# Performance work log

Hardware: AMD Instinct MI355X
Metric: run time of the kernel (lower is better)

## Reference

```python
import jax, jax.numpy as jnp
import numpy as np

H = 2048
S = 8192

def setup_inputs() -> dict:
    key = jax.random.key(0)
    k1, k2, k3 = jax.random.split(key, 3)
    hidden = jax.random.normal(k1, (1, 1, H), dtype=jnp.float32)
    encoder_outputs = jax.random.normal(k2, (S, 1, H), dtype=jnp.float32)
    # nn.Linear(H, H): weight [H, H], bias [H]; Kaiming-uniform-ish scale
    bound = 1.0 / np.sqrt(H)
    W = jax.random.uniform(k3, (H, H), dtype=jnp.float32, minval=-bound, maxval=bound)
    b = jnp.zeros((H,), dtype=jnp.float32)
    return {"hidden": hidden, "encoder_outputs": encoder_outputs, "W": W, "b": b}

def reference(hidden, encoder_outputs, W, b):
    # hidden: [1,1,H] -> [H]; encoder_outputs: [S,1,H] -> [S,H]
    h = hidden[0, 0]
    enc = encoder_outputs[:, 0, :]
    # per-step: energy_i = W @ enc_i + b; score_i = h . energy_i  (vectorized)
    energies = jnp.einsum('sh,h->s', enc @ W.T + b, h)  # [S]
    attn = jax.nn.softmax(energies)  # softmax over seq dim (dim 0 of 1-D tensor)
    return attn[None, None, :]  # [1,1,S]
```

## Files before the change

kernel.cpp:

```cpp
#include <hip/hip_runtime.h>
#include <math.h>

#define H 2048
#define S 8192
#define JCHUNK 64

__global__ void wt_h_kernel(const float* __restrict__ W, const float* __restrict__ h,
                            float* __restrict__ u) {
    int k = blockIdx.x * blockDim.x + threadIdx.x;
    int j0 = blockIdx.y * JCHUNK;
    float acc = 0.f;
#pragma unroll 8
    for (int j = j0; j < j0 + JCHUNK; ++j) {
        acc += h[j] * W[(size_t)j * H + k];
    }
    atomicAdd(&u[k], acc);
}

__global__ void enc_dot_kernel(const float* __restrict__ enc, const float* __restrict__ u,
                               float* __restrict__ e) {
    int wave = threadIdx.x >> 6;
    int lane = threadIdx.x & 63;
    int s = blockIdx.x * 4 + wave;
    const float4* row = (const float4*)(enc + (size_t)s * H);
    const float4* u4  = (const float4*)u;
    float acc = 0.f;
#pragma unroll
    for (int i = lane; i < H / 4; i += 64) {
        float4 a = row[i];
        float4 b = u4[i];
        acc += a.x * b.x + a.y * b.y + a.z * b.z + a.w * b.w;
    }
#pragma unroll
    for (int off = 32; off > 0; off >>= 1) acc += __shfl_down(acc, off);
    if (lane == 0) e[s] = acc;
}

__global__ void softmax_kernel(const float* __restrict__ e, float* __restrict__ out) {
    __shared__ float red[16];
    __shared__ float bcast;
    int tid = threadIdx.x;
    int lane = tid & 63;
    int wv = tid >> 6;

    float vals[8];
    float m = -INFINITY;
#pragma unroll
    for (int i = 0; i < 8; ++i) {
        vals[i] = e[tid + i * 1024];
        m = fmaxf(m, vals[i]);
    }
#pragma unroll
    for (int off = 32; off > 0; off >>= 1) m = fmaxf(m, __shfl_down(m, off));
    if (lane == 0) red[wv] = m;
    __syncthreads();
    if (tid == 0) {
        float mm = red[0];
#pragma unroll
        for (int i = 1; i < 16; ++i) mm = fmaxf(mm, red[i]);
        bcast = mm;
    }
    __syncthreads();
    float M = bcast;

    float ssum = 0.f;
#pragma unroll
    for (int i = 0; i < 8; ++i) {
        vals[i] = __expf(vals[i] - M);
        ssum += vals[i];
    }
#pragma unroll
    for (int off = 32; off > 0; off >>= 1) ssum += __shfl_down(ssum, off);
    if (lane == 0) red[wv] = ssum;
    __syncthreads();
    if (tid == 0) {
        float t = 0.f;
#pragma unroll
        for (int i = 0; i < 16; ++i) t += red[i];
        bcast = t;
    }
    __syncthreads();
    float inv = 1.f / bcast;
#pragma unroll
    for (int i = 0; i < 8; ++i) out[tid + i * 1024] = vals[i] * inv;
}

extern "C" void kernel_launch(void* const* d_in, const int* in_sizes, int n_in,
                              void* d_out, int out_size, void* d_ws, size_t ws_size,
                              hipStream_t stream) {
    const float* hidden = (const float*)d_in[0];
    const float* enc    = (const float*)d_in[1];
    const float* W      = (const float*)d_in[2];
    float* out = (float*)d_out;

    float* u = (float*)d_ws;
    float* e = (float*)((char*)d_ws + H * sizeof(float));

    hipMemsetAsync(u, 0, H * sizeof(float), stream);

    dim3 g1(H / 256, H / JCHUNK);
    wt_h_kernel<<<g1, 256, 0, stream>>>(W, hidden, u);

    enc_dot_kernel<<<S / 4, 256, 0, stream>>>(enc, u, e);

    softmax_kernel<<<1, 1024, 0, stream>>>(e, out);
}
```

Before: 114.2 us.

## Fuse all stages into one cooperative kernel with grid syncs and online softmax

Replaces the memset plus three kernel launches with a single cooperative kernel of 1024 blocks. Stage one computes partial W^T·h slices into a buffer, avoiding atomics; a second stage reduces them. Each block then computes 8 encoder dot products and a local max and exp-sum, and a final stage combines all block partials to normalise. This removes launch gaps and the single-block softmax, at the cost of three grid-wide barriers and a co-residency requirement (falls back to the old path if the cooperative launch fails).

New measurement: 411.6 us. 3.6x slower.

```diff
diff --git a/kernel.cpp b/kernel.cpp
--- a/kernel.cpp
+++ b/kernel.cpp
@@ -1,8 +1,116 @@
 #include <hip/hip_runtime.h>
+#include <hip/hip_cooperative_groups.h>
 #include <math.h>
 
 #define H 2048
 #define S 8192
+#define NBLK 1024
+#define NSLICE 128
+#define JCH (H / NSLICE)
+
+namespace cg = cooperative_groups;
+
+__global__ __launch_bounds__(256, 4)
+void fused_attn(const float* __restrict__ W, const float* __restrict__ h,
+                const float* __restrict__ enc, float* __restrict__ out,
+                float* __restrict__ u_part, float* __restrict__ u,
+                float* __restrict__ red) {
+    cg::grid_group grid = cg::this_grid();
+    const int b    = blockIdx.x;
+    const int tid  = threadIdx.x;
+    const int lane = tid & 63;
+    const int wave = tid >> 6;
+
+    __shared__ float evals[8];
+    __shared__ float wred[4];
+    __shared__ float bc[2];
+
+    {
+        const int kx = b & 7;
+        const int js = b >> 3;
+        const int k  = kx * 256 + tid;
+        const int j0 = js * JCH;
+        float acc = 0.f;
+#pragma unroll
+        for (int j = j0; j < j0 + JCH; ++j)
+            acc += h[j] * W[(size_t)j * H + k];
+        u_part[(size_t)js * H + k] = acc;
+    }
+    grid.sync();
+
+    {
+        const int t = b * 256 + tid;
+        if (t < H) {
+            float acc = 0.f;
+#pragma unroll 8
+            for (int js = 0; js < NSLICE; ++js)
+                acc += u_part[(size_t)js * H + t];
+            u[t] = acc;
+        }
+    }
+    grid.sync();
+
+    {
+        const float4* u4 = (const float4*)u;
+        for (int r = wave; r < 8; r += 4) {
+            const int s = b * 8 + r;
+            const float4* row = (const float4*)(enc + (size_t)s * H);
+            float acc = 0.f;
+#pragma unroll
+            for (int it = 0; it < 8; ++it) {
+                float4 a  = row[lane + it * 64];
+                float4 bb = u4 [lane + it * 64];
+                acc += a.x * bb.x + a.y * bb.y + a.z * bb.z + a.w * bb.w;
+            }
+#pragma unroll
+            for (int off = 32; off > 0; off >>= 1) acc += __shfl_down(acc, off);
+            if (lane == 0) evals[r] = acc;
+        }
+        __syncthreads();
+        if (tid == 0) {
+            float m = evals[0];
+#pragma unroll
+            for (int i = 1; i < 8; ++i) m = fmaxf(m, evals[i]);
+            float sb = 0.f;
+#pragma unroll
+            for (int i = 0; i < 8; ++i) sb += __expf(evals[i] - m);
+            red[2 * b]     = m;
+            red[2 * b + 1] = sb;
+        }
+    }
+    grid.sync();
+
+    {
+        float m4[4], s4[4];
+        float mt = -INFINITY;
+#pragma unroll
+        for (int q = 0; q < 4; ++q) {
+            const int i = tid + q * 256;
+            m4[q] = red[2 * i];
+            s4[q] = red[2 * i + 1];
+            mt = fmaxf(mt, m4[q]);
+        }
+#pragma unroll
+        for (int off = 32; off > 0; off >>= 1) mt = fmaxf(mt, __shfl_down(mt, off));
+        if (lane == 0) wred[wave] = mt;
+        __syncthreads();
+        if (tid == 0) bc[0] = fmaxf(fmaxf(wred[0], wred[1]), fmaxf(wred[2], wred[3]));
+        __syncthreads();
+        const float M = bc[0];
+        float st = 0.f;
+#pragma unroll
+        for (int q = 0; q < 4; ++q) st += s4[q] * __expf(m4[q] - M);
+#pragma unroll
+        for (int off = 32; off > 0; off >>= 1) st += __shfl_down(st, off);
+        if (lane == 0) wred[wave] = st;
+        __syncthreads();
+        if (tid == 0) bc[1] = wred[0] + wred[1] + wred[2] + wred[3];
+        __syncthreads();
+        const float inv = 1.f / bc[1];
+        if (tid < 8) out[b * 8 + tid] = __expf(evals[tid] - M) * inv;
+    }
+}
+
 #define JCHUNK 64
 
 __global__ void wt_h_kernel(const float* __restrict__ W, const float* __restrict__ h,
@@ -11,9 +119,7 @@
     int j0 = blockIdx.y * JCHUNK;
     float acc = 0.f;
 #pragma unroll 8
-    for (int j = j0; j < j0 + JCHUNK; ++j) {
-        acc += h[j] * W[(size_t)j * H + k];
-    }
+    for (int j = j0; j < j0 + JCHUNK; ++j) acc += h[j] * W[(size_t)j * H + k];
     atomicAdd(&u[k], acc);
 }
 
@@ -42,14 +148,10 @@
     int tid = threadIdx.x;
     int lane = tid & 63;
     int wv = tid >> 6;
-
     float vals[8];
     float m = -INFINITY;
 #pragma unroll
-    for (int i = 0; i < 8; ++i) {
-        vals[i] = e[tid + i * 1024];
-        m = fmaxf(m, vals[i]);
-    }
+    for (int i = 0; i < 8; ++i) { vals[i] = e[tid + i * 1024]; m = fmaxf(m, vals[i]); }
 #pragma unroll
     for (int off = 32; off > 0; off >>= 1) m = fmaxf(m, __shfl_down(m, off));
     if (lane == 0) red[wv] = m;
@@ -62,13 +164,9 @@
     }
     __syncthreads();
     float M = bcast;
-
     float ssum = 0.f;
 #pragma unroll
-    for (int i = 0; i < 8; ++i) {
-        vals[i] = __expf(vals[i] - M);
-        ssum += vals[i];
-    }
+    for (int i = 0; i < 8; ++i) { vals[i] = __expf(vals[i] - M); ssum += vals[i]; }
 #pragma unroll
     for (int off = 32; off > 0; off >>= 1) ssum += __shfl_down(ssum, off);
     if (lane == 0) red[wv] = ssum;
@@ -93,15 +191,21 @@
     const float* W      = (const float*)d_in[2];
     float* out = (float*)d_out;
 
-    float* u = (float*)d_ws;
-    float* e = (float*)((char*)d_ws + H * sizeof(float));
-
-    hipMemsetAsync(u, 0, H * sizeof(float), stream);
-
-    dim3 g1(H / 256, H / JCHUNK);
-    wt_h_kernel<<<g1, 256, 0, stream>>>(W, hidden, u);
-
-    enc_dot_kernel<<<S / 4, 256, 0, stream>>>(enc, u, e);
-
-    softmax_kernel<<<1, 1024, 0, stream>>>(e, out);
-}
+    float* u_part = (float*)d_ws;
+    float* u      = u_part + (size_t)NSLICE * H;
+    float* red    = u + H;
+
+    void* args[] = { (void*)&W, (void*)&hidden, (void*)&enc, (void*)&out,
+                     (void*)&u_part, (void*)&u, (void*)&red };
+    hipError_t err = hipLaunchCooperativeKernel((void*)fused_attn,
+                                                dim3(NBLK), dim3(256),
+                                                args, 0, stream);
+    if (err != hipSuccess) {
+        float* e = red;
+        hipMemsetAsync(u, 0, H * sizeof(float), stream);
+        dim3 g1(H / 256, H / JCHUNK);
+        wt_h_kernel<<<g1, 256, 0, stream>>>(W, hidden, u);
+        enc_dot_kernel<<<S / 4, 256, 0, stream>>>(enc, u, e);
+        softmax_kernel<<<1, 1024, 0, stream>>>(e, out);
+    }
+}
```

## Split softmax into per-block partial reductions and parallel finalize, vectorize W^T h

Applied to the files above, without the earlier changes.

The enc_dot kernel now writes a per-block max and sum-of-exponentials, and a 32-block finalize kernel combines these partials and normalizes the outputs in parallel. This replaces the single-block 1024-thread softmax, which serialized the tail of the pipeline. The W^T h kernel now loads float4 and uses smaller j-chunks (16), giving 256 blocks and four times as many atomics. Each finalize block redundantly re-reads all 2048 partial pairs.

Result: slower. 125.3 us (+9.7%).

```diff
diff --git a/kernel.cpp b/kernel.cpp
--- a/kernel.cpp
+++ b/kernel.cpp
@@ -3,86 +3,98 @@
 
 #define H 2048
 #define S 8192
-#define JCHUNK 64
+#define KJ 16
 
-__global__ void wt_h_kernel(const float* __restrict__ W, const float* __restrict__ h,
-                            float* __restrict__ u) {
-    int k = blockIdx.x * blockDim.x + threadIdx.x;
-    int j0 = blockIdx.y * JCHUNK;
-    float acc = 0.f;
-#pragma unroll 8
-    for (int j = j0; j < j0 + JCHUNK; ++j) {
-        acc += h[j] * W[(size_t)j * H + k];
+__global__ __launch_bounds__(256)
+void wt_h_kernel(const float* __restrict__ W, const float* __restrict__ h,
+                 float* __restrict__ u) {
+    const int k4 = blockIdx.x * 256 + threadIdx.x;
+    const int j0 = blockIdx.y * KJ;
+    const float4* W4 = (const float4*)W;
+    float4 acc = make_float4(0.f, 0.f, 0.f, 0.f);
+#pragma unroll
+    for (int j = j0; j < j0 + KJ; ++j) {
+        const float hv = h[j];
+        const float4 w = W4[(size_t)j * (H / 4) + k4];
+        acc.x += hv * w.x; acc.y += hv * w.y;
+        acc.z += hv * w.z; acc.w += hv * w.w;
     }
-    atomicAdd(&u[k], acc);
+    float* up = u + 4 * (size_t)k4;
+    atomicAdd(up + 0, acc.x);
+    atomicAdd(up + 1, acc.y);
+    atomicAdd(up + 2, acc.z);
+    atomicAdd(up + 3, acc.w);
 }
 
-__global__ void enc_dot_kernel(const float* __restrict__ enc, const float* __restrict__ u,
-                               float* __restrict__ e) {
-    int wave = threadIdx.x >> 6;
-    int lane = threadIdx.x & 63;
-    int s = blockIdx.x * 4 + wave;
+__global__ __launch_bounds__(256)
+void enc_dot_kernel(const float* __restrict__ enc, const float* __restrict__ u,
+                    float* __restrict__ e, float* __restrict__ red) {
+    __shared__ float ev[4];
+    const int wave = threadIdx.x >> 6;
+    const int lane = threadIdx.x & 63;
+    const int s = blockIdx.x * 4 + wave;
     const float4* row = (const float4*)(enc + (size_t)s * H);
     const float4* u4  = (const float4*)u;
     float acc = 0.f;
 #pragma unroll
-    for (int i = lane; i < H / 4; i += 64) {
-        float4 a = row[i];
-        float4 b = u4[i];
+    for (int it = 0; it < 8; ++it) {
+        const float4 a = row[lane + 64 * it];
+        const float4 b = u4 [lane + 64 * it];
         acc += a.x * b.x + a.y * b.y + a.z * b.z + a.w * b.w;
     }
 #pragma unroll
     for (int off = 32; off > 0; off >>= 1) acc += __shfl_down(acc, off);
-    if (lane == 0) e[s] = acc;
+    if (lane == 0) { e[s] = acc; ev[wave] = acc; }
+    __syncthreads();
+    if (threadIdx.x == 0) {
+        float m = fmaxf(fmaxf(ev[0], ev[1]), fmaxf(ev[2], ev[3]));
+        float sb = 0.f;
+#pragma unroll
+        for (int i = 0; i < 4; ++i) sb += __expf(ev[i] - m);
+        red[2 * blockIdx.x]     = m;
+        red[2 * blockIdx.x + 1] = sb;
+    }
 }
 
-__global__ void softmax_kernel(const float* __restrict__ e, float* __restrict__ out) {
-    __shared__ float red[16];
-    __shared__ float bcast;
-    int tid = threadIdx.x;
-    int lane = tid & 63;
-    int wv = tid >> 6;
+__global__ __launch_bounds__(256)
+void finalize_kernel(const float* __restrict__ e, const float* __restrict__ red,
+                     float* __restrict__ out) {
+    __shared__ float wred[4];
+    __shared__ float bc[2];
+    const int tid = threadIdx.x;
+    const int lane = tid & 63;
+    const int wave = tid >> 6;
+    const float2* pr = (const float2*)red;
 
-    float vals[8];
-    float m = -INFINITY;
+    float m8[8], s8[8];
+    float mt = -INFINITY;
 #pragma unroll
-    for (int i = 0; i < 8; ++i) {
-        vals[i] = e[tid + i * 1024];
-        m = fmaxf(m, vals[i]);
+    for (int q = 0; q < 8; ++q) {
+        const float2 p = pr[tid + 256 * q];
+        m8[q] = p.x; s8[q] = p.y;
+        mt = fmaxf(mt, p.x);
     }
 #pragma unroll
-    for (int off = 32; off > 0; off >>= 1) m = fmaxf(m, __shfl_down(m, off));
-    if (lane == 0) red[wv] = m;
+    for (int off = 32; off > 0; off >>= 1) mt = fmaxf(mt, __shfl_down(mt, off));
+    if (lane == 0) wred[wave] = mt;
     __syncthreads();
-    if (tid == 0) {
-        float mm = red[0];
+    if (tid == 0) bc[0] = fmaxf(fmaxf(wred[0], wred[1]), fmaxf(wred[2], wred[3]));
+    __syncthreads();
+    const float M = bc[0];
+
+    float st = 0.f;
 #pragma unroll
-        for (int i = 1; i < 16; ++i) mm = fmaxf(mm, red[i]);
-        bcast = mm;
-    }
+    for (int q = 0; q < 8; ++q) st += s8[q] * __expf(m8[q] - M);
+#pragma unroll
+    for (int off = 32; off > 0; off >>= 1) st += __shfl_down(st, off);
+    if (lane == 0) wred[wave] = st;
     __syncthreads();
-    float M = bcast;
+    if (tid == 0) bc[1] = wred[0] + wred[1] + wred[2] + wred[3];
+    __syncthreads();
+    const float inv = 1.f / bc[1];
 
-    float ssum = 0.f;
-#pragma unroll
-    for (int i = 0; i < 8; ++i) {
-        vals[i] = __expf(vals[i] - M);
-        ssum += vals[i];
-    }
-#pragma unroll
-    for (int off = 32; off > 0; off >>= 1) ssum += __shfl_down(ssum, off);
-    if (lane == 0) red[wv] = ssum;
-    __syncthreads();
-    if (tid == 0) {
-        float t = 0.f;
-#pragma unroll
-        for (int i = 0; i < 16; ++i) t += red[i];
-        bcast = t;
-    }
-    __syncthreads();
-    float inv = 1.f / bcast;
-#pragma unroll
-    for (int i = 0; i < 8; ++i) out[tid + i * 1024] = vals[i] * inv;
+    const int i = blockIdx.x * 256 + tid;
+    out[i] = __expf(e[i] - M) * inv;
 }
 
 extern "C" void kernel_launch(void* const* d_in, const int* in_sizes, int n_in,
@@ -93,15 +105,15 @@
     const float* W      = (const float*)d_in[2];
     float* out = (float*)d_out;
 
-    float* u = (float*)d_ws;
-    float* e = (float*)((char*)d_ws + H * sizeof(float));
+    float* u   = (float*)d_ws;
+    float* e   = u + H;
+    float* red = e + S;
 
     hipMemsetAsync(u, 0, H * sizeof(float), stream);
 
-    dim3 g1(H / 256, H / JCHUNK);
-    wt_h_kernel<<<g1, 256, 0, stream>>>(W, hidden, u);
+    wt_h_kernel<<<dim3(H / 1024, H / KJ), 256, 0, stream>>>(W, hidden, u);
 
-    enc_dot_kernel<<<S / 4, 256, 0, stream>>>(enc, u, e);
+    enc_dot_kernel<<<S / 4, 256, 0, stream>>>(enc, u, e, red);
 
-    softmax_kernel<<<1, 1024, 0, stream>>>(e, out);
+    finalize_kernel<<<S / 256, 256, 0, stream>>>(e, red, out);
 }
```
